# Performance work log

Hardware: AMD Instinct MI355X
Metric: run time of the kernel (lower is better)

Reference implementation:

```python
import jax, jax.numpy as jnp
import numpy as np

N, E, D, R, L = 100000, 800000, 64, 7, 3
HID, KH = D // 4, 32          # IEConv hidden = dims[i]//4, kernel_hidden_dim = 32
EDGE_DIM = 14
BN_EPS = 1e-5
LN_EPS = 1e-5


def _normalize(v, eps=1e-12):
    n = jnp.linalg.norm(v, axis=-1, keepdims=True)
    return v / jnp.maximum(n, eps)


def _bn(h, p):
    # eval-mode BatchNorm1d; p: [4, dim] = (gamma, beta, running_mean, running_var)
    return (h - p[2]) * jax.lax.rsqrt(p[3] + BN_EPS) * p[0] + p[1]


def setup_inputs() -> dict:
    key = jax.random.key(0)
    keys = iter(jax.random.split(key, 40))
    nk = lambda: next(keys)
    par = lambda shape, s=0.1: jax.random.normal(nk(), shape, jnp.float32) * s

    def bn_par(dim):
        g = 1.0 + 0.1 * jax.random.normal(nk(), (L, dim), jnp.float32)
        b = 0.1 * jax.random.normal(nk(), (L, dim), jnp.float32)
        m = 0.1 * jax.random.normal(nk(), (L, dim), jnp.float32)
        v = 0.5 + jax.random.uniform(nk(), (L, dim), jnp.float32)
        return jnp.stack([g, b, m, v], axis=1)  # [L,4,dim]

    inp = {
        "x": jax.random.normal(nk(), (N, D), jnp.float32),
        "pos": jax.random.normal(nk(), (N, 3), jnp.float32) * 10.0,
        "edge_index": jax.random.randint(nk(), (2, E), 0, N),
        "edge_relation": jax.random.randint(nk(), (E,), 0, R),
        # GeometricRelationalGraphConv params (per layer)
        "W_rel": par((L, R * D, D)), "b_rel": par((L, D)),
        "W_self": par((L, D, D)), "b_self": par((L, D)),
        # IEConvLayer params
        "W_l1": par((L, D, HID)), "b_l1": par((L, HID)),
        "W_k1": par((L, EDGE_DIM, KH)), "b_k1": par((L, KH)),
        "W_k2": par((L, KH, (HID + 1) * HID)), "b_k2": par((L, (HID + 1) * HID)),
        "W_l2": par((L, HID, D)), "b_l2": par((L, D)),
        "bn_in": bn_par(D), "bn_msg": bn_par(HID), "bn_upd": bn_par(HID), "bn_out": bn_par(D),
        "ln_g": 1.0 + 0.1 * jax.random.normal(nk(), (L, D), jnp.float32),
        "ln_b": 0.1 * jax.random.normal(nk(), (L, D), jnp.float32),
    }
    return inp


def _forward(x, pos, W_rel, b_rel, W_self, b_self, W_l1, b_l1, W_k1, b_k1,
             W_k2, b_k2, W_l2, b_l2, bn_in, bn_msg, bn_upd, bn_out, ln_g, ln_b,
             edge_index, edge_relation):
    node_in, node_out = edge_index[0], edge_index[1]
    # ---- get_ieconv_edge_feature ----
    ones3 = jnp.ones((1, 3), x.dtype)
    u = _normalize(jnp.concatenate([ones3, pos[1:] - pos[:-1]], axis=0))        # [N,3]
    b = _normalize(jnp.concatenate([u[:-1] - u[1:], ones3], axis=0))
    n = _normalize(jnp.concatenate([jnp.cross(u[:-1], u[1:]), ones3], axis=0))
    frame = jnp.stack([b, n, jnp.cross(b, n)], axis=-1)                          # [N,3,3]
    t = jnp.einsum('ejk,ej->ek', frame[node_in], pos[node_out] - pos[node_in])  # [E,3]
    r = jnp.sum(frame[node_in] * frame[node_out], axis=1)                        # [E,3]
    delta = (jnp.abs(node_in - node_out).astype(x.dtype) / 6.0)[:, None]         # atom2residue = arange
    edge_feat = jnp.concatenate(
        [t, r, delta, 1 - 2 * jnp.abs(t), 1 - 2 * jnp.abs(r), 1 - 2 * jnp.abs(delta)], axis=-1)  # [E,14]

    deg = jnp.maximum(
        jax.ops.segment_sum(jnp.ones_like(node_out, dtype=x.dtype), node_out, num_segments=N), 1.0)[:, None]
    seg = node_out * R + edge_relation
    h = x
    for i in range(L):
        # GeometricRelationalGraphConv: relation-bucketed scatter-sum, per-relation linear + self loop, relu
        upd = jax.ops.segment_sum(h[node_in], seg, num_segments=N * R).reshape(N, R * h.shape[-1])
        rel_out = jax.nn.relu(upd @ W_rel[i] + b_rel[i] + h @ W_self[i] + b_self[i])
        # IEConvLayer (eval mode, dropouts identity)
        li = jax.nn.relu(_bn(h, bn_in[i]))
        m = jax.nn.relu(_bn(li[node_in] @ W_l1[i] + b_l1[i], bn_msg[i]))         # [E,HID]
        ker = (jax.nn.relu(edge_feat @ W_k1[i] + b_k1[i]) @ W_k2[i] + b_k2[i]).reshape(-1, HID + 1, HID)
        m = jnp.einsum('ejk,ej->ek', ker[:, 1:, :], m) + ker[:, 0, :]            # per-edge kernel conv
        upd2 = jax.ops.segment_sum(m, node_out, num_segments=N) / deg            # scatter-mean
        upd2 = jax.nn.relu(_bn(upd2, bn_upd[i]))
        ie_out = _bn(upd2 @ W_l2[i] + b_l2[i], bn_out[i])
        hidden = rel_out + ie_out + h  # short_cut: shapes match at every layer
        mu = jnp.mean(hidden, axis=-1, keepdims=True)
        var = jnp.var(hidden, axis=-1, keepdims=True)
        h = (hidden - mu) * jax.lax.rsqrt(var + LN_EPS) * ln_g[i] + ln_b[i]
    return h


def reference(x, pos, edge_index, edge_relation, W_rel, b_rel, W_self, b_self,
              W_l1, b_l1, W_k1, b_k1, W_k2, b_k2, W_l2, b_l2,
              bn_in, bn_msg, bn_upd, bn_out, ln_g, ln_b):
    return _forward(x, pos, W_rel, b_rel, W_self, b_self, W_l1, b_l1, W_k1, b_k1,
                    W_k2, b_k2, W_l2, b_l2, bn_in, bn_msg, bn_upd, bn_out, ln_g, ln_b,
                    edge_index, edge_relation)
```

## Files before the change

### kernel.cpp

```cpp
#include <hip/hip_runtime.h>
#include <hip/hip_bf16.h>

typedef unsigned short u16;
typedef unsigned int   u32;

static const int Nn  = 100000;
static const int Ne  = 800000;
static const int Ll  = 3;
static const int SCAN_B = 98;

typedef short     short8  __attribute__((ext_vector_type(8)));
typedef float     floatx4 __attribute__((ext_vector_type(4)));

static const int H_CUM[19] = {
  0, 86016, 86208, 98496, 98688, 101760, 101808, 103152, 103248,
  129360, 130176, 133248, 133440, 134208, 134400, 134592, 135360, 135552, 135744
};
static const int H_SZ[18] = {
  86016, 192, 12288, 192, 3072, 48, 1344, 96,
  26112, 816, 3072, 192, 768, 192, 192, 768, 192, 192
};

union FU { u32 u; float f; };
__device__ __forceinline__ float b2f(u16 v) { FU x; x.u = ((u32)v) << 16; return x.f; }
__device__ __forceinline__ float lo2f(u32 w) { FU x; x.u = w << 16; return x.f; }
__device__ __forceinline__ float hi2f(u32 w) { FU x; x.u = w & 0xffff0000u; return x.f; }
__device__ __forceinline__ u16 f2b(float f) {
  FU x; x.f = f;
  u32 u = x.u;
  u32 r = (u + 0x7FFFu + ((u >> 16) & 1u)) >> 16;
  return (u16)r;
}
__device__ __forceinline__ u32 pk2(float a, float b) {
  __hip_bfloat162 h2 = __float22bfloat162_rn(make_float2(a, b));
  union { __hip_bfloat162 h; u32 u; } c; c.h = h2; return c.u;
}

__global__ void k_bnprep(const float* __restrict__ W, float* __restrict__ bnAB) {
  int idx = blockIdx.x * blockDim.x + threadIdx.x;
  if (idx >= 480) return;
  int i = idx / 160, d0 = idx % 160;
  const float* src; float* dstA; float* dstB; int dim, d;
  if (d0 < 64)       { d = d0;      src = W + 133440 + i * 256; dim = 64; dstA = bnAB + i*320 + 0;   dstB = bnAB + i*320 + 64;  }
  else if (d0 < 80)  { d = d0 - 64; src = W + 134208 + i * 64;  dim = 16; dstA = bnAB + i*320 + 128; dstB = bnAB + i*320 + 144; }
  else if (d0 < 96)  { d = d0 - 80; src = W + 134400 + i * 64;  dim = 16; dstA = bnAB + i*320 + 160; dstB = bnAB + i*320 + 176; }
  else               { d = d0 - 96; src = W + 134592 + i * 256; dim = 64; dstA = bnAB + i*320 + 192; dstB = bnAB + i*320 + 256; }
  float g = src[0*dim+d], b = src[1*dim+d], m = src[2*dim+d], v = src[3*dim+d];
  float A = g * rsqrtf(v + 1e-5f);
  float B = b - m * A;
  dstA[d] = A; dstB[d] = B;
}

__global__ void k_prep(const float* __restrict__ W, u16* __restrict__ BswG) {
  int i = blockIdx.x * 256 + threadIdx.x;
  if (i >= 3 * 8704) return;
  int layer = i / 8704, r = i % 8704;
  int jp = r / 512, l2 = r % 512;
  int lane = l2 / 8, j = l2 % 8;
  int q = (lane >> 4) * 8 + j, n = lane & 15;
  const float* Wk2 = W + 103248 + layer * 8704;
  BswG[i] = f2b(Wk2[q * 272 + jp * 16 + n]);
}

__global__ void k_prep2(const float* __restrict__ W, u16* __restrict__ B3) {
  int idx = blockIdx.x * 256 + threadIdx.x;
  if (idx >= 3 * 65536) return;
  int layer = idx >> 16, r = idx & 65535;
  int fr = r >> 9;
  int lane = (r >> 3) & 63, j = r & 7;
  int nt = fr & 3, hl = (fr >> 2) & 1, ks = fr >> 3;
  int k = ks * 32 + (lane >> 4) * 8 + j;
  int g = nt * 16 + (lane & 15);
  const float* Wrel  = W + layer * 28672;
  const float* Wself = W + 86208 + layer * 4096;
  float v = (k < 448) ? Wrel[k * 64 + g] : Wself[(k - 448) * 64 + g];
  u16 hi = f2b(v);
  B3[idx] = hl ? f2b(v - b2f(hi)) : hi;
}

__global__ void k_prep3(const float* __restrict__ W, u16* __restrict__ Wk1f) {
  int idx = blockIdx.x * 256 + threadIdx.x;
  if (idx >= 3 * 2048) return;
  int layer = idx / 2048, r = idx % 2048;
  int kind = (r >> 10) & 1, nt = (r >> 9) & 1;
  int lane = (r >> 3) & 63, j = r & 7;
  int k = (lane >> 4) * 8 + j;
  int q = nt * 16 + (lane & 15);
  const float* Wk1 = W + 101808 + layer * 448;
  u16 out = 0;
  if (kind == 0) {
    if (k < 14)       out = f2b(Wk1[k * 32 + q]);
    else if (k < 28)  out = f2b(Wk1[(k - 14) * 32 + q]);
  } else {
    if (k < 14) {
      float w = Wk1[k * 32 + q];
      u16 hi = f2b(w);
      out = f2b(w - b2f(hi));
    }
  }
  Wk1f[idx] = out;
}

__global__ void k_u(const float* __restrict__ posf, float* __restrict__ u) {
  int i = blockIdx.x * blockDim.x + threadIdx.x;
  if (i >= Nn) return;
  float ux, uy, uz;
  if (i == 0) { ux = uy = uz = 0.57735026918962584f; }
  else {
    float vx = posf[i*3+0] - posf[(i-1)*3+0];
    float vy = posf[i*3+1] - posf[(i-1)*3+1];
    float vz = posf[i*3+2] - posf[(i-1)*3+2];
    float nrm = sqrtf(vx*vx + vy*vy + vz*vz);
    float inv = 1.0f / fmaxf(nrm, 1e-12f);
    ux = vx*inv; uy = vy*inv; uz = vz*inv;
  }
  u[i*3+0] = ux; u[i*3+1] = uy; u[i*3+2] = uz;
}

__global__ void k_frame(const float* __restrict__ u, float* __restrict__ frame) {
  int i = blockIdx.x * blockDim.x + threadIdx.x;
  if (i >= Nn) return;
  float bx, by, bz, nx, ny, nz;
  if (i < Nn - 1) {
    float ax = u[i*3+0], ay = u[i*3+1], az = u[i*3+2];
    float cx = u[(i+1)*3+0], cy = u[(i+1)*3+1], cz = u[(i+1)*3+2];
    float dx = ax-cx, dy = ay-cy, dz = az-cz;
    float n1 = sqrtf(dx*dx + dy*dy + dz*dz);
    float i1 = 1.0f / fmaxf(n1, 1e-12f);
    bx = dx*i1; by = dy*i1; bz = dz*i1;
    float qx = ay*cz - az*cy, qy = az*cx - ax*cz, qz = ax*cy - ay*cx;
    float n2 = sqrtf(qx*qx + qy*qy + qz*qz);
    float i2 = 1.0f / fmaxf(n2, 1e-12f);
    nx = qx*i2; ny = qy*i2; nz = qz*i2;
  } else {
    bx = by = bz = 0.57735026918962584f;
    nx = ny = nz = 0.57735026918962584f;
  }
  float ex = by*nz - bz*ny, ey = bz*nx - bx*nz, ez = bx*ny - by*nx;
  frame[i*9+0] = bx; frame[i*9+1] = nx; frame[i*9+2] = ex;
  frame[i*9+3] = by; frame[i*9+4] = ny; frame[i*9+5] = ey;
  frame[i*9+6] = bz; frame[i*9+7] = nz; frame[i*9+8] = ez;
}

__global__ void k_edge(const int* __restrict__ EI, const float* __restrict__ posf,
                       const float* __restrict__ frame,
                       float* __restrict__ t0, float* __restrict__ t1, float* __restrict__ t2,
                       float* __restrict__ r0, float* __restrict__ r1, float* __restrict__ r2,
                       int* __restrict__ cnt) {
  int e = blockIdx.x * 256 + threadIdx.x;
  int vin = EI[e], vout = EI[Ne + e];
  float fi[9], fo[9];
#pragma unroll
  for (int t = 0; t < 9; t++) fi[t] = frame[(size_t)vin*9 + t];
#pragma unroll
  for (int t = 0; t < 9; t++) fo[t] = frame[(size_t)vout*9 + t];
  float d0 = posf[vout*3+0] - posf[vin*3+0];
  float d1 = posf[vout*3+1] - posf[vin*3+1];
  float d2 = posf[vout*3+2] - posf[vin*3+2];
  float tt[3], rr[3];
#pragma unroll
  for (int k = 0; k < 3; k++) {
    tt[k] = fi[0*3+k]*d0 + fi[1*3+k]*d1 + fi[2*3+k]*d2;
    rr[k] = fi[0*3+k]*fo[0*3+k] + fi[1*3+k]*fo[1*3+k] + fi[2*3+k]*fo[2*3+k];
  }
  t0[e] = tt[0]; t1[e] = tt[1]; t2[e] = tt[2];
  r0[e] = rr[0]; r1[e] = rr[1]; r2[e] = rr[2];
  atomicAdd(&cnt[vout], 1);
}

__global__ __launch_bounds__(1024) void k_scan1(const int* __restrict__ cnt,
                                                int* __restrict__ locExc,
                                                int* __restrict__ btot) {
  __shared__ int sm[1024];
  int t = threadIdx.x, b = blockIdx.x;
  int i = b * 1024 + t;
  int v = (i < Nn) ? cnt[i] : 0;
  sm[t] = v;
  __syncthreads();
#pragma unroll
  for (int off = 1; off < 1024; off <<= 1) {
    int x = (t >= off) ? sm[t - off] : 0;
    __syncthreads();
    sm[t] += x;
    __syncthreads();
  }
  if (i < Nn) locExc[i] = sm[t] - v;
  if (t == 1023) btot[b] = sm[1023];
}

__global__ void k_scan2(const int* __restrict__ btot, int* __restrict__ boff,
                        int* __restrict__ rowptr) {
  if (threadIdx.x != 0 || blockIdx.x != 0) return;
  int run = 0;
  for (int b = 0; b < SCAN_B; b++) { boff[b] = run; run += btot[b]; }
  rowptr[Nn] = run;
}

__global__ void k_scan3(const int* __restrict__ cnt, const int* __restrict__ locExc,
                        const int* __restrict__ boff, int* __restrict__ rowptr,
                        float* __restrict__ deginv) {
  int i = blockIdx.x * blockDim.x + threadIdx.x;
  if (i >= Nn) return;
  rowptr[i] = locExc[i] + boff[i >> 10];
  int dv = cnt[i] > 1 ? cnt[i] : 1;
  deginv[i] = 1.0f / (float)dv;
}

__global__ void k_place(const int* __restrict__ EI, const int* __restrict__ EREL,
                        const int* __restrict__ rowptr,
                        int* __restrict__ fill, int* __restrict__ yidx,
                        int* __restrict__ inv) {
  int e = blockIdx.x * blockDim.x + threadIdx.x;
  if (e >= Ne) return;
  int vout = EI[Ne + e];
  int p = atomicAdd(&fill[vout], 1);
  int slot = rowptr[vout] + p;
  inv[e] = slot;
  yidx[slot] = EI[e] * 8 + EREL[e];
}

__global__ __launch_bounds__(256) void k_z(
    const float* __restrict__ h, const float* __restrict__ Wl1, const float* __restrict__ bl1,
    const float* __restrict__ bk2, const float* __restrict__ bn,
    u16* __restrict__ zt, u16* __restrict__ biast, u16* __restrict__ h16) {
  __shared__ float ls[64][65];
  __shared__ float zz[64][17];
  int tid = threadIdx.x;
  int nb0 = blockIdx.x * 64;
  const float* Ain = bn + 0;
  const float* Bin = bn + 64;
#pragma unroll
  for (int r = 0; r < 16; r++) {
    int idx = r * 256 + tid;
    int row = idx >> 6, col = idx & 63;
    int node = nb0 + row;
    float v = (node < Nn) ? h[(size_t)node * 64 + col] : 0.0f;
    if (node < Nn) h16[(size_t)node * 64 + col] = f2b(v);
    ls[row][col] = fmaxf(v * Ain[col] + Bin[col], 0.0f);
  }
  __syncthreads();
  int row = tid >> 2, jq = (tid & 3) * 4;
  int node = nb0 + row;
  const float* Amsg = bn + 128;
  const float* Bmsg = bn + 144;
  float m1[4];
#pragma unroll
  for (int t = 0; t < 4; t++) m1[t] = bl1[jq + t];
  for (int c = 0; c < 64; c++) {
    float lv = ls[row][c];
#pragma unroll
    for (int t = 0; t < 4; t++) m1[t] += lv * Wl1[c * 16 + jq + t];
  }
  float zv[4];
#pragma unroll
  for (int t = 0; t < 4; t++) {
    zv[t] = fmaxf(m1[t] * Amsg[jq + t] + Bmsg[jq + t], 0.0f);
    zz[row][jq + t] = zv[t];
  }
  if (node < Nn) {
    u32* zg = (u32*)zt + (size_t)node * 8 + (tid & 3) * 2;
    zg[0] = pk2(zv[0], zv[1]);
    zg[1] = pk2(zv[2], zv[3]);
  }
  __syncthreads();
  float bb[4];
#pragma unroll
  for (int t = 0; t < 4; t++) bb[t] = bk2[jq + t];
  for (int j = 0; j < 16; j++) {
    float zj = zz[row][j];
#pragma unroll
    for (int t = 0; t < 4; t++) bb[t] += zj * bk2[(j + 1) * 16 + jq + t];
  }
  if (node < Nn) {
    u32* bg = (u32*)biast + (size_t)node * 8 + (tid & 3) * 2;
    bg[0] = pk2(bb[0], bb[1]);
    bg[1] = pk2(bb[2], bb[3]);
  }
}

__global__ __launch_bounds__(256) void k_relagg(
    const float* __restrict__ h, const u16* __restrict__ h16,
    const int* __restrict__ rowptr, const int* __restrict__ yidx,
    const u16* __restrict__ Bsw3,
    const float* __restrict__ brel, const float* __restrict__ bself,
    u16* __restrict__ rel16) {
  __shared__ __align__(16) u16 uh[16][520];
  __shared__ __align__(16) u16 ul[16][520];
  int tid = threadIdx.x;
  int w = tid >> 6, lane = tid & 63;
  int grp = lane >> 4, cl = lane & 15;
  int nb0 = blockIdx.x * 16;
  int anode = nb0 + w * 4 + grp;
  int lrow = w * 4 + grp;
  union U { uint4 u; short8 v; };

  float acc[7][4];
#pragma unroll
  for (int r = 0; r < 7; r++)
#pragma unroll
    for (int c = 0; c < 4; c++) acc[r][c] = 0.0f;
  if (anode < Nn) {
    int beg = rowptr[anode], end = rowptr[anode + 1];
    for (int p = beg; p < end; p++) {
      int ye = yidx[p];
      int vin = ye >> 3, rl = ye & 7;
      uint2 d = *(const uint2*)(h16 + (size_t)vin * 64 + cl * 4);
      float v0 = lo2f(d.x), v1 = hi2f(d.x), v2 = lo2f(d.y), v3 = hi2f(d.y);
#pragma unroll
      for (int r = 0; r < 7; r++) {
        bool hit = (rl == r);
        acc[r][0] += hit ? v0 : 0.0f;
        acc[r][1] += hit ? v1 : 0.0f;
        acc[r][2] += hit ? v2 : 0.0f;
        acc[r][3] += hit ? v3 : 0.0f;
      }
    }
  }
#pragma unroll
  for (int r = 0; r < 7; r++) {
#pragma unroll
    for (int c = 0; c < 4; c++) {
      float v = acc[r][c];
      u16 hi = f2b(v);
      uh[lrow][r * 64 + cl * 4 + c] = hi;
      ul[lrow][r * 64 + cl * 4 + c] = f2b(v - b2f(hi));
    }
  }
  {
    float q[4] = {0.f, 0.f, 0.f, 0.f};
    if (anode < Nn) {
      float4 hv = ((const float4*)(h + (size_t)anode * 64))[cl];
      q[0] = hv.x; q[1] = hv.y; q[2] = hv.z; q[3] = hv.w;
    }
#pragma unroll
    for (int c = 0; c < 4; c++) {
      u16 hi = f2b(q[c]);
      uh[lrow][448 + cl * 4 + c] = hi;
      ul[lrow][448 + cl * 4 + c] = f2b(q[c] - b2f(hi));
    }
  }
  __syncthreads();

  int quad = lane >> 4;
  floatx4 o4 = {0.f, 0.f, 0.f, 0.f};
  const u16* B0 = Bsw3 + (size_t)w * 512 + lane * 8;
#pragma unroll
  for (int ks = 0; ks < 16; ks++) {
    U ah, al, bh, bl;
    ah.u = *(const uint4*)(&uh[cl][ks * 32 + quad * 8]);
    al.u = *(const uint4*)(&ul[cl][ks * 32 + quad * 8]);
    bh.u = *(const uint4*)(B0 + (size_t)(ks * 2 + 0) * 2048);
    bl.u = *(const uint4*)(B0 + (size_t)(ks * 2 + 1) * 2048);
    o4 = __builtin_amdgcn_mfma_f32_16x16x32_bf16(ah.v, bh.v, o4, 0, 0, 0);
    o4 = __builtin_amdgcn_mfma_f32_16x16x32_bf16(al.v, bh.v, o4, 0, 0, 0);
    o4 = __builtin_amdgcn_mfma_f32_16x16x32_bf16(ah.v, bl.v, o4, 0, 0, 0);
  }
  int g = w * 16 + cl;
  float bias = brel[g] + bself[g];
#pragma unroll
  for (int reg = 0; reg < 4; reg++) {
    int node = nb0 + quad * 4 + reg;
    if (node < Nn)
      rel16[(size_t)node * 64 + g] = f2b(fmaxf(o4[reg] + bias, 0.0f));
  }
}

__global__ __launch_bounds__(256) void k_msg(
    const float* __restrict__ t0, const float* __restrict__ t1, const float* __restrict__ t2,
    const float* __restrict__ r0, const float* __restrict__ r1, const float* __restrict__ r2,
    const int* __restrict__ EI, const int* __restrict__ inv,
    const u16* __restrict__ zt, const u16* __restrict__ biast,
    const u16* __restrict__ Wk1f, const float* __restrict__ bk1,
    const u16* __restrict__ BswG, u16* __restrict__ mo) {
  __shared__ u16 abuf[256 * 40];
  __shared__ u32 bsw[4352];
  __shared__ int ivin[256];

  int tid = threadIdx.x;
  int e0 = blockIdx.x * 256;
  int e = e0 + tid;

  for (int i = tid; i < 4352; i += 256) bsw[i] = ((const u32*)BswG)[i];

  int vin = EI[e], vout = EI[Ne + e];
  ivin[tid] = vin;

  float ef[14];
  ef[0] = t0[e]; ef[1] = t1[e]; ef[2] = t2[e];
  ef[3] = r0[e]; ef[4] = r1[e]; ef[5] = r2[e];
  int ad = vin - vout; if (ad < 0) ad = -ad;
  ef[6] = ((float)ad) / 6.0f;
#pragma unroll
  for (int k = 0; k < 7; k++) ef[7+k] = 1.0f - 2.0f*fabsf(ef[k]);

  u16 row[32];
#pragma unroll
  for (int d = 0; d < 14; d++) {
    u16 hi = f2b(ef[d]);
    row[d] = hi;
    row[14 + d] = f2b(ef[d] - b2f(hi));
  }
#pragma unroll
  for (int d = 28; d < 32; d++) row[d] = 0;
  u32* ar = (u32*)(abuf + (size_t)tid * 40);
#pragma unroll
  for (int i = 0; i < 16; i++)
    ar[i] = (u32)row[2*i] | ((u32)row[2*i+1] << 16);
  __syncthreads();

  int lane = tid & 63, w4 = (tid >> 6) * 4;
  int m = lane & 15, quad = lane >> 4;
  union U { uint4 u; short8 v; };

  U b0[2], b1[2];
#pragma unroll
  for (int nt = 0; nt < 2; nt++) {
    b0[nt].u = *(const uint4*)(Wk1f + 0*1024 + nt*512 + lane*8);
    b1[nt].u = *(const uint4*)(Wk1f + 1*1024 + nt*512 + lane*8);
  }
  float bk1v[2] = { bk1[m], bk1[16 + m] };

#pragma unroll
  for (int t = 0; t < 4; t++) {
    int s0 = (w4 + t) * 16;
    const u16* rs0 = abuf + (size_t)(s0 + m) * 40;

    U efr; efr.u = *(const uint4*)(rs0 + quad * 8);
#pragma unroll
    for (int nt = 0; nt < 2; nt++) {
      floatx4 aa = {0.f, 0.f, 0.f, 0.f};
      aa = __builtin_amdgcn_mfma_f32_16x16x32_bf16(efr.v, b0[nt].v, aa, 0, 0, 0);
      aa = __builtin_amdgcn_mfma_f32_16x16x32_bf16(efr.v, b1[nt].v, aa, 0, 0, 0);
#pragma unroll
      for (int reg = 0; reg < 4; reg++) {
        int se = s0 + quad * 4 + reg;
        float av = fmaxf(aa[reg] + bk1v[nt], 0.0f);
        abuf[(size_t)se * 40 + nt * 16 + m] = f2b(av);
      }
    }
    U afr; afr.u = *(const uint4*)(rs0 + quad * 8);

    int se0 = s0 + quad * 4;
    uint4 z0[4], z1[4]; float bv[4]; int sl[4];
#pragma unroll
    for (int reg = 0; reg < 4; reg++) {
      int vi = ivin[se0 + reg];
      const uint4* zp = (const uint4*)(zt + (size_t)vi * 16);
      z0[reg] = zp[0]; z1[reg] = zp[1];
      bv[reg] = b2f(biast[(size_t)vi * 16 + m]);
      sl[reg] = inv[e0 + se0 + reg];
    }

    float acc[4];
    {
      U bfr; bfr.u = *(const uint4*)(bsw + (size_t)lane * 4);
      floatx4 zz4 = {0.f, 0.f, 0.f, 0.f};
      floatx4 k0 = __builtin_amdgcn_mfma_f32_16x16x32_bf16(afr.v, bfr.v, zz4, 0, 0, 0);
#pragma unroll
      for (int reg = 0; reg < 4; reg++) acc[reg] = k0[reg];
    }
#pragma unroll
    for (int jp = 1; jp <= 16; jp++) {
      U bfr; bfr.u = *(const uint4*)(bsw + (size_t)(jp * 64 + lane) * 4);
      floatx4 zz4 = {0.f, 0.f, 0.f, 0.f};
      floatx4 kj = __builtin_amdgcn_mfma_f32_16x16x32_bf16(afr.v, bfr.v, zz4, 0, 0, 0);
      const int zi = jp - 1;
#pragma unroll
      for (int reg = 0; reg < 4; reg++) {
        const u32* zw = (zi < 8) ? (const u32*)&z0[reg] : (const u32*)&z1[reg];
        u32 wv = zw[(zi & 7) >> 1];
        float zv = (zi & 1) ? hi2f(wv) : lo2f(wv);
        acc[reg] += zv * kj[reg];
      }
    }
#pragma unroll
    for (int reg = 0; reg < 4; reg++)
      mo[(size_t)sl[reg] * 16 + m] = f2b(acc[reg] + bv[reg]);
  }
}

__global__ __launch_bounds__(256) void k_node(
    const float* __restrict__ h, const u16* __restrict__ rel16,
    const int* __restrict__ rowptr,
    const u16* __restrict__ mo, const float* __restrict__ deginv,
    const float* __restrict__ Wl2, const float* __restrict__ bl2,
    const float* __restrict__ bn, const float* __restrict__ lng, const float* __restrict__ lnb,
    float* __restrict__ hout) {
  __shared__ float u2s[4][16];
  int tid = threadIdx.x;
  int lane = tid & 63, w = tid >> 6;
  int n = blockIdx.x * 4 + w;
  bool act = (n < Nn);

  if (act) {
    int beg = rowptr[n], end = rowptr[n+1];
    int r = lane >> 2, c4 = lane & 3;
    float p4[4] = {0.f, 0.f, 0.f, 0.f};
    for (int p0 = beg; p0 < end; p0 += 16) {
      int p = p0 + r;
      if (p < end) {
        uint2 d = *(const uint2*)(mo + (size_t)p * 16 + c4 * 4);
        p4[0] += lo2f(d.x); p4[1] += hi2f(d.x);
        p4[2] += lo2f(d.y); p4[3] += hi2f(d.y);
      }
    }
#pragma unroll
    for (int t = 0; t < 4; t++) {
      p4[t] += __shfl_xor(p4[t],  4, 64);
      p4[t] += __shfl_xor(p4[t],  8, 64);
      p4[t] += __shfl_xor(p4[t], 16, 64);
      p4[t] += __shfl_xor(p4[t], 32, 64);
    }
    const float* Aupd = bn + 160;
    const float* Bupd = bn + 176;
    if (lane < 4) {
      float di = deginv[n];
#pragma unroll
      for (int t = 0; t < 4; t++) {
        int col = c4 * 4 + t;
        float v = p4[t] * di;
        u2s[w][col] = fmaxf(v * Aupd[col] + Bupd[col], 0.0f);
      }
    }
  }
  __syncthreads();
  if (act) {
    float rel_out = b2f(rel16[(size_t)n*64 + lane]);
    float ie = bl2[lane];
#pragma unroll
    for (int j = 0; j < 16; j++) ie += u2s[w][j] * Wl2[j*64 + lane];
    const float* Aout = bn + 192;
    const float* Bout = bn + 256;
    ie = ie * Aout[lane] + Bout[lane];
    float hidden = rel_out + ie + h[(size_t)n*64 + lane];
    float s = hidden;
#pragma unroll
    for (int off = 32; off > 0; off >>= 1) s += __shfl_xor(s, off, 64);
    float mu = s * (1.0f/64.0f);
    float d = hidden - mu;
    float s2 = d * d;
#pragma unroll
    for (int off = 32; off > 0; off >>= 1) s2 += __shfl_xor(s2, off, 64);
    float var = s2 * (1.0f/64.0f);
    float o = d * rsqrtf(var + 1e-5f) * lng[lane] + lnb[lane];
    hout[(size_t)n*64 + lane] = o;
  }
}

extern "C" void kernel_launch(void* const* d_in, const int* in_sizes, int n_in,
                              void* d_out, int out_size, void* d_ws, size_t ws_size,
                              hipStream_t stream) {
  const float* x    = (const float*)d_in[0];
  const float* posf = (const float*)d_in[1];
  const int* EI     = (const int*)d_in[2];
  const int* EREL   = (const int*)d_in[3];
  float* outf       = (float*)d_out;

  char* p = (char*)d_ws;
  auto alloc = [&](size_t bytes) -> char* {
    char* r = p;
    p += (bytes + 255) & ~((size_t)255);
    return r;
  };
  float* W      = (float*)alloc((size_t)135744 * 4);
  float* bnAB   = (float*)alloc((size_t)960 * 4);
  u16*   BswG   = (u16*)  alloc((size_t)3 * 8704 * 2);
  u16*   Bsw3   = (u16*)  alloc((size_t)3 * 65536 * 2);
  u16*   Wk1f   = (u16*)  alloc((size_t)3 * 2048 * 2);
  float* u      = (float*)alloc((size_t)Nn * 3 * 4);
  float* frame  = (float*)alloc((size_t)Nn * 9 * 4);
  int*   cnt    = (int*)  alloc((size_t)Nn * 4);
  int*   fill   = (int*)  alloc((size_t)Nn * 4);
  int*   rowptr = (int*)  alloc((size_t)(Nn + 1) * 4);
  int*   locExc = (int*)  alloc((size_t)Nn * 4);
  int*   btot   = (int*)  alloc((size_t)SCAN_B * 4);
  int*   boff   = (int*)  alloc((size_t)SCAN_B * 4);
  int*   yidx   = (int*)  alloc((size_t)Ne * 4);
  int*   inv    = (int*)  alloc((size_t)Ne * 4);
  float* deginv = (float*)alloc((size_t)Nn * 4);
  float* h      = (float*)alloc((size_t)Nn * 64 * 4);
  u16*   h16    = (u16*)  alloc((size_t)Nn * 64 * 2);
  u16*   rel16  = (u16*)  alloc((size_t)Nn * 64 * 2);
  u16*   mo     = (u16*)  alloc((size_t)Ne * 16 * 2);
  u16*   zt     = (u16*)  alloc((size_t)Nn * 16 * 2);
  u16*   biast  = (u16*)  alloc((size_t)Nn * 16 * 2);
  float* et0    = (float*)alloc((size_t)Ne * 4);
  float* et1    = (float*)alloc((size_t)Ne * 4);
  float* et2    = (float*)alloc((size_t)Ne * 4);
  float* er0    = (float*)alloc((size_t)Ne * 4);
  float* er1    = (float*)alloc((size_t)Ne * 4);
  float* er2    = (float*)alloc((size_t)Ne * 4);
  (void)n_in; (void)in_sizes; (void)out_size;

  size_t needed = (size_t)(p - (char*)d_ws);
  if (needed > ws_size) return;

  hipMemsetAsync(cnt,  0, (size_t)Nn * 4, stream);
  hipMemsetAsync(fill, 0, (size_t)Nn * 4, stream);

  for (int k = 0; k < 18; k++)
    hipMemcpyAsync(W + H_CUM[k], d_in[4 + k], (size_t)H_SZ[k] * 4,
                   hipMemcpyDeviceToDevice, stream);
  hipMemcpyAsync(h, x, (size_t)Nn * 64 * 4, hipMemcpyDeviceToDevice, stream);

  k_bnprep<<<2, 256, 0, stream>>>(W, bnAB);
  k_prep<<<(3*8704 + 255)/256, 256, 0, stream>>>(W, BswG);
  k_prep2<<<(3*65536 + 255)/256, 256, 0, stream>>>(W, Bsw3);
  k_prep3<<<(3*2048 + 255)/256, 256, 0, stream>>>(W, Wk1f);
  k_u<<<(Nn + 255)/256, 256, 0, stream>>>(posf, u);
  k_frame<<<(Nn + 255)/256, 256, 0, stream>>>(u, frame);
  k_edge<<<Ne/256, 256, 0, stream>>>(EI, posf, frame, et0, et1, et2, er0, er1, er2, cnt);
  k_scan1<<<SCAN_B, 1024, 0, stream>>>(cnt, locExc, btot);
  k_scan2<<<1, 64, 0, stream>>>(btot, boff, rowptr);
  k_scan3<<<(Nn + 255)/256, 256, 0, stream>>>(cnt, locExc, boff, rowptr, deginv);
  k_place<<<Ne/256, 256, 0, stream>>>(EI, EREL, rowptr, fill, yidx, inv);

  for (int i = 0; i < Ll; i++) {
    const float* brel  = W + H_CUM[1]  + i * 64;
    const float* bself = W + H_CUM[3]  + i * 64;
    const float* Wl1   = W + H_CUM[4]  + i * 1024;
    const float* bl1   = W + H_CUM[5]  + i * 16;
    const float* bk1   = W + H_CUM[7]  + i * 32;
    const float* bk2   = W + H_CUM[9]  + i * 272;
    const float* Wl2   = W + H_CUM[10] + i * 1024;
    const float* bl2   = W + H_CUM[11] + i * 64;
    const float* lng   = W + H_CUM[16] + i * 64;
    const float* lnb   = W + H_CUM[17] + i * 64;
    const float* bnL   = bnAB + i * 320;
    const u16*   BswL  = BswG + i * 8704;

    k_z<<<(Nn + 63)/64, 256, 0, stream>>>(h, Wl1, bl1, bk2, bnL, zt, biast, h16);
    k_relagg<<<(Nn + 15)/16, 256, 0, stream>>>(h, h16, rowptr, yidx,
                                               Bsw3 + i * 65536, brel, bself, rel16);
    k_msg<<<Ne/256, 256, 0, stream>>>(et0, et1, et2, er0, er1, er2, EI, inv,
                                      zt, biast, Wk1f + i * 2048, bk1, BswL, mo);
    k_node<<<(Nn + 3)/4, 256, 0, stream>>>(h, rel16, rowptr, mo, deginv,
                                           Wl2, bl2, bnL, lng, lnb,
                                           (i == Ll - 1) ? outf : h);
  }
}
```

Measured before the change: 947.6 us.

## Sort CSR edges by (destination, relation) to drop per-relation predicated accumulation

```diff
diff --git a/kernel.cpp b/kernel.cpp
--- a/kernel.cpp
+++ b/kernel.cpp
@@ -7,7 +7,7 @@
 static const int Nn  = 100000;
 static const int Ne  = 800000;
 static const int Ll  = 3;
-static const int SCAN_B = 98;
+static const int SCAN_B8 = 782;
 
 typedef short     short8  __attribute__((ext_vector_type(8)));
 typedef float     floatx4 __attribute__((ext_vector_type(4)));
@@ -142,11 +142,12 @@
   frame[i*9+6] = bz; frame[i*9+7] = nz; frame[i*9+8] = ez;
 }
 
-__global__ void k_edge(const int* __restrict__ EI, const float* __restrict__ posf,
+__global__ void k_edge(const int* __restrict__ EI, const int* __restrict__ EREL,
+                       const float* __restrict__ posf,
                        const float* __restrict__ frame,
                        float* __restrict__ t0, float* __restrict__ t1, float* __restrict__ t2,
                        float* __restrict__ r0, float* __restrict__ r1, float* __restrict__ r2,
-                       int* __restrict__ cnt) {
+                       int* __restrict__ cnt8) {
   int e = blockIdx.x * 256 + threadIdx.x;
   int vin = EI[e], vout = EI[Ne + e];
   float fi[9], fo[9];
@@ -165,16 +166,16 @@
   }
   t0[e] = tt[0]; t1[e] = tt[1]; t2[e] = tt[2];
   r0[e] = rr[0]; r1[e] = rr[1]; r2[e] = rr[2];
-  atomicAdd(&cnt[vout], 1);
-}
-
-__global__ __launch_bounds__(1024) void k_scan1(const int* __restrict__ cnt,
+  atomicAdd(&cnt8[(size_t)vout * 8 + EREL[e]], 1);
+}
+
+__global__ __launch_bounds__(1024) void k_scan1(const int* __restrict__ cnt8,
                                                 int* __restrict__ locExc,
                                                 int* __restrict__ btot) {
   __shared__ int sm[1024];
   int t = threadIdx.x, b = blockIdx.x;
   int i = b * 1024 + t;
-  int v = (i < Nn) ? cnt[i] : 0;
+  int v = (i < Nn * 8) ? cnt8[i] : 0;
   sm[t] = v;
   __syncthreads();
 #pragma unroll
@@ -184,39 +185,44 @@
     sm[t] += x;
     __syncthreads();
   }
-  if (i < Nn) locExc[i] = sm[t] - v;
+  if (i < Nn * 8) locExc[i] = sm[t] - v;
   if (t == 1023) btot[b] = sm[1023];
 }
 
 __global__ void k_scan2(const int* __restrict__ btot, int* __restrict__ boff,
-                        int* __restrict__ rowptr) {
+                        int* __restrict__ rp8) {
   if (threadIdx.x != 0 || blockIdx.x != 0) return;
   int run = 0;
-  for (int b = 0; b < SCAN_B; b++) { boff[b] = run; run += btot[b]; }
-  rowptr[Nn] = run;
-}
-
-__global__ void k_scan3(const int* __restrict__ cnt, const int* __restrict__ locExc,
-                        const int* __restrict__ boff, int* __restrict__ rowptr,
-                        float* __restrict__ deginv) {
+  for (int b = 0; b < SCAN_B8; b++) { boff[b] = run; run += btot[b]; }
+  rp8[Nn * 8] = run;
+}
+
+__global__ void k_scan3(const int* __restrict__ cnt8, const int* __restrict__ locExc,
+                        const int* __restrict__ boff, int* __restrict__ rp8) {
+  int i = blockIdx.x * blockDim.x + threadIdx.x;
+  if (i >= Nn * 8) return;
+  rp8[i] = locExc[i] + boff[i >> 10];
+}
+
+__global__ void k_deg(const int* __restrict__ rp8, float* __restrict__ deginv) {
   int i = blockIdx.x * blockDim.x + threadIdx.x;
   if (i >= Nn) return;
-  rowptr[i] = locExc[i] + boff[i >> 10];
-  int dv = cnt[i] > 1 ? cnt[i] : 1;
-  deginv[i] = 1.0f / (float)dv;
+  int d = rp8[i * 8 + 8] - rp8[i * 8];
+  deginv[i] = 1.0f / (float)(d > 1 ? d : 1);
 }
 
 __global__ void k_place(const int* __restrict__ EI, const int* __restrict__ EREL,
-                        const int* __restrict__ rowptr,
-                        int* __restrict__ fill, int* __restrict__ yidx,
+                        const int* __restrict__ rp8,
+                        int* __restrict__ fill8, int* __restrict__ yidx,
                         int* __restrict__ inv) {
   int e = blockIdx.x * blockDim.x + threadIdx.x;
   if (e >= Ne) return;
   int vout = EI[Ne + e];
-  int p = atomicAdd(&fill[vout], 1);
-  int slot = rowptr[vout] + p;
+  int idx8 = vout * 8 + EREL[e];
+  int p = atomicAdd(&fill8[idx8], 1);
+  int slot = rp8[idx8] + p;
   inv[e] = slot;
-  yidx[slot] = EI[e] * 8 + EREL[e];
+  yidx[slot] = EI[e];
 }
 
 __global__ __launch_bounds__(256) void k_z(
@@ -280,64 +286,57 @@
 
 __global__ __launch_bounds__(256) void k_relagg(
     const float* __restrict__ h, const u16* __restrict__ h16,
-    const int* __restrict__ rowptr, const int* __restrict__ yidx,
+    const int* __restrict__ rp8, const int* __restrict__ yidx,
     const u16* __restrict__ Bsw3,
     const float* __restrict__ brel, const float* __restrict__ bself,
     u16* __restrict__ rel16) {
-  __shared__ __align__(16) u16 uh[16][520];
-  __shared__ __align__(16) u16 ul[16][520];
+  __shared__ __align__(16) u16 uh[16 * 528];
+  __shared__ __align__(16) u16 ul[16 * 528];
   int tid = threadIdx.x;
   int w = tid >> 6, lane = tid & 63;
   int grp = lane >> 4, cl = lane & 15;
   int nb0 = blockIdx.x * 16;
   int anode = nb0 + w * 4 + grp;
   int lrow = w * 4 + grp;
+  bool act = (anode < Nn);
   union U { uint4 u; short8 v; };
 
-  float acc[7][4];
-#pragma unroll
-  for (int r = 0; r < 7; r++)
-#pragma unroll
-    for (int c = 0; c < 4; c++) acc[r][c] = 0.0f;
-  if (anode < Nn) {
-    int beg = rowptr[anode], end = rowptr[anode + 1];
-    for (int p = beg; p < end; p++) {
-      int ye = yidx[p];
-      int vin = ye >> 3, rl = ye & 7;
-      uint2 d = *(const uint2*)(h16 + (size_t)vin * 64 + cl * 4);
-      float v0 = lo2f(d.x), v1 = hi2f(d.x), v2 = lo2f(d.y), v3 = hi2f(d.y);
-#pragma unroll
-      for (int r = 0; r < 7; r++) {
-        bool hit = (rl == r);
-        acc[r][0] += hit ? v0 : 0.0f;
-        acc[r][1] += hit ? v1 : 0.0f;
-        acc[r][2] += hit ? v2 : 0.0f;
-        acc[r][3] += hit ? v3 : 0.0f;
+  int ksb = cl >> 3;
+  int qk  = (cl & 7) >> 1;
+  int j0  = (cl & 1) * 4;
+  int wbase = (qk * 16 + lrow) * 8 + j0;
+
+#pragma unroll
+  for (int r = 0; r < 7; r++) {
+    float a0 = 0.f, a1 = 0.f, a2 = 0.f, a3 = 0.f;
+    if (act) {
+      int b8 = rp8[anode * 8 + r], e8 = rp8[anode * 8 + r + 1];
+      for (int p = b8; p < e8; p++) {
+        int vin = yidx[p];
+        uint2 d = *(const uint2*)(h16 + (size_t)vin * 64 + cl * 4);
+        a0 += lo2f(d.x); a1 += hi2f(d.x);
+        a2 += lo2f(d.y); a3 += hi2f(d.y);
       }
     }
-  }
-#pragma unroll
-  for (int r = 0; r < 7; r++) {
-#pragma unroll
-    for (int c = 0; c < 4; c++) {
-      float v = acc[r][c];
-      u16 hi = f2b(v);
-      uh[lrow][r * 64 + cl * 4 + c] = hi;
-      ul[lrow][r * 64 + cl * 4 + c] = f2b(v - b2f(hi));
-    }
+    int ks = 2 * r + ksb;
+    u16 h0 = f2b(a0), h1 = f2b(a1), h2 = f2b(a2), h3 = f2b(a3);
+    *(uint2*)(uh + ks * 528 + wbase) =
+        make_uint2((u32)h0 | ((u32)h1 << 16), (u32)h2 | ((u32)h3 << 16));
+    *(uint2*)(ul + ks * 528 + wbase) =
+        make_uint2(pk2(a0 - b2f(h0), a1 - b2f(h1)), pk2(a2 - b2f(h2), a3 - b2f(h3)));
   }
   {
-    float q[4] = {0.f, 0.f, 0.f, 0.f};
-    if (anode < Nn) {
+    float q0 = 0.f, q1 = 0.f, q2 = 0.f, q3 = 0.f;
+    if (act) {
       float4 hv = ((const float4*)(h + (size_t)anode * 64))[cl];
-      q[0] = hv.x; q[1] = hv.y; q[2] = hv.z; q[3] = hv.w;
-    }
-#pragma unroll
-    for (int c = 0; c < 4; c++) {
-      u16 hi = f2b(q[c]);
-      uh[lrow][448 + cl * 4 + c] = hi;
-      ul[lrow][448 + cl * 4 + c] = f2b(q[c] - b2f(hi));
-    }
+      q0 = hv.x; q1 = hv.y; q2 = hv.z; q3 = hv.w;
+    }
+    int ks = 14 + ksb;
+    u16 h0 = f2b(q0), h1 = f2b(q1), h2 = f2b(q2), h3 = f2b(q3);
+    *(uint2*)(uh + ks * 528 + wbase) =
+        make_uint2((u32)h0 | ((u32)h1 << 16), (u32)h2 | ((u32)h3 << 16));
+    *(uint2*)(ul + ks * 528 + wbase) =
+        make_uint2(pk2(q0 - b2f(h0), q1 - b2f(h1)), pk2(q2 - b2f(h2), q3 - b2f(h3)));
   }
   __syncthreads();
 
@@ -347,8 +346,8 @@
 #pragma unroll
   for (int ks = 0; ks < 16; ks++) {
     U ah, al, bh, bl;
-    ah.u = *(const uint4*)(&uh[cl][ks * 32 + quad * 8]);
-    al.u = *(const uint4*)(&ul[cl][ks * 32 + quad * 8]);
+    ah.u = *(const uint4*)(uh + ks * 528 + lane * 8);
+    al.u = *(const uint4*)(ul + ks * 528 + lane * 8);
     bh.u = *(const uint4*)(B0 + (size_t)(ks * 2 + 0) * 2048);
     bl.u = *(const uint4*)(B0 + (size_t)(ks * 2 + 1) * 2048);
     o4 = __builtin_amdgcn_mfma_f32_16x16x32_bf16(ah.v, bh.v, o4, 0, 0, 0);
@@ -481,7 +480,7 @@
 
 __global__ __launch_bounds__(256) void k_node(
     const float* __restrict__ h, const u16* __restrict__ rel16,
-    const int* __restrict__ rowptr,
+    const int* __restrict__ rp8,
     const u16* __restrict__ mo, const float* __restrict__ deginv,
     const float* __restrict__ Wl2, const float* __restrict__ bl2,
     const float* __restrict__ bn, const float* __restrict__ lng, const float* __restrict__ lnb,
@@ -493,7 +492,7 @@
   bool act = (n < Nn);
 
   if (act) {
-    int beg = rowptr[n], end = rowptr[n+1];
+    int beg = rp8[n * 8], end = rp8[n * 8 + 8];
     int r = lane >> 2, c4 = lane & 3;
     float p4[4] = {0.f, 0.f, 0.f, 0.f};
     for (int p0 = beg; p0 < end; p0 += 16) {
@@ -569,12 +568,12 @@
   u16*   Wk1f   = (u16*)  alloc((size_t)3 * 2048 * 2);
   float* u      = (float*)alloc((size_t)Nn * 3 * 4);
   float* frame  = (float*)alloc((size_t)Nn * 9 * 4);
-  int*   cnt    = (int*)  alloc((size_t)Nn * 4);
-  int*   fill   = (int*)  alloc((size_t)Nn * 4);
-  int*   rowptr = (int*)  alloc((size_t)(Nn + 1) * 4);
-  int*   locExc = (int*)  alloc((size_t)Nn * 4);
-  int*   btot   = (int*)  alloc((size_t)SCAN_B * 4);
-  int*   boff   = (int*)  alloc((size_t)SCAN_B * 4);
+  int*   cnt8   = (int*)  alloc((size_t)Nn * 8 * 4);
+  int*   fill8  = (int*)  alloc((size_t)Nn * 8 * 4);
+  int*   rp8    = (int*)  alloc((size_t)(Nn * 8 + 8) * 4);
+  int*   locExc = (int*)  alloc((size_t)Nn * 8 * 4);
+  int*   btot   = (int*)  alloc((size_t)SCAN_B8 * 4);
+  int*   boff   = (int*)  alloc((size_t)SCAN_B8 * 4);
   int*   yidx   = (int*)  alloc((size_t)Ne * 4);
   int*   inv    = (int*)  alloc((size_t)Ne * 4);
   float* deginv = (float*)alloc((size_t)Nn * 4);
@@ -595,8 +594,8 @@
   size_t needed = (size_t)(p - (char*)d_ws);
   if (needed > ws_size) return;
 
-  hipMemsetAsync(cnt,  0, (size_t)Nn * 4, stream);
-  hipMemsetAsync(fill, 0, (size_t)Nn * 4, stream);
+  hipMemsetAsync(cnt8,  0, (size_t)Nn * 8 * 4, stream);
+  hipMemsetAsync(fill8, 0, (size_t)Nn * 8 * 4, stream);
 
   for (int k = 0; k < 18; k++)
     hipMemcpyAsync(W + H_CUM[k], d_in[4 + k], (size_t)H_SZ[k] * 4,
@@ -609,11 +608,12 @@
   k_prep3<<<(3*2048 + 255)/256, 256, 0, stream>>>(W, Wk1f);
   k_u<<<(Nn + 255)/256, 256, 0, stream>>>(posf, u);
   k_frame<<<(Nn + 255)/256, 256, 0, stream>>>(u, frame);
-  k_edge<<<Ne/256, 256, 0, stream>>>(EI, posf, frame, et0, et1, et2, er0, er1, er2, cnt);
-  k_scan1<<<SCAN_B, 1024, 0, stream>>>(cnt, locExc, btot);
-  k_scan2<<<1, 64, 0, stream>>>(btot, boff, rowptr);
-  k_scan3<<<(Nn + 255)/256, 256, 0, stream>>>(cnt, locExc, boff, rowptr, deginv);
-  k_place<<<Ne/256, 256, 0, stream>>>(EI, EREL, rowptr, fill, yidx, inv);
+  k_edge<<<Ne/256, 256, 0, stream>>>(EI, EREL, posf, frame, et0, et1, et2, er0, er1, er2, cnt8);
+  k_scan1<<<SCAN_B8, 1024, 0, stream>>>(cnt8, locExc, btot);
+  k_scan2<<<1, 64, 0, stream>>>(btot, boff, rp8);
+  k_scan3<<<(Nn * 8 + 255)/256, 256, 0, stream>>>(cnt8, locExc, boff, rp8);
+  k_deg<<<(Nn + 255)/256, 256, 0, stream>>>(rp8, deginv);
+  k_place<<<Ne/256, 256, 0, stream>>>(EI, EREL, rp8, fill8, yidx, inv);
 
   for (int i = 0; i < Ll; i++) {
     const float* brel  = W + H_CUM[1]  + i * 64;
@@ -630,11 +630,11 @@
     const u16*   BswL  = BswG + i * 8704;
 
     k_z<<<(Nn + 63)/64, 256, 0, stream>>>(h, Wl1, bl1, bk2, bnL, zt, biast, h16);
-    k_relagg<<<(Nn + 15)/16, 256, 0, stream>>>(h, h16, rowptr, yidx,
+    k_relagg<<<(Nn + 15)/16, 256, 0, stream>>>(h, h16, rp8, yidx,
                                                Bsw3 + i * 65536, brel, bself, rel16);
     k_msg<<<Ne/256, 256, 0, stream>>>(et0, et1, et2, er0, er1, er2, EI, inv,
                                       zt, biast, Wk1f + i * 2048, bk1, BswL, mo);
-    k_node<<<(Nn + 3)/4, 256, 0, stream>>>(h, rel16, rowptr, mo, deginv,
+    k_node<<<(Nn + 3)/4, 256, 0, stream>>>(h, rel16, rp8, mo, deginv,
                                            Wl2, bl2, bnL, lng, lnb,
                                            (i == Ll - 1) ? outf : h);
   }
```

After: 1.027 ms. 8.3% more time.
